# Kernel optimization log

Measured on AMD Instinct MI355X. Metric: run time of the kernel, lower is better.

Reference implementation:

```python
import jax, jax.numpy as jnp
import numpy as np

B, C, H, W = 4, 96, 64, 64
N_STATE, DT_RANK, K = 16, 6, 3


def _layernorm(x, g, b, eps=1e-5):
    m = jnp.mean(x, axis=-1, keepdims=True)
    v = jnp.mean((x - m) ** 2, axis=-1, keepdims=True)
    return (x - m) / jnp.sqrt(v + eps) * g + b


def _grid_sample(img, gx, gy):
    # F.grid_sample: bilinear, align_corners=True, zeros padding; gx,gy in [-1,1], [B,Ho,Wo]
    Bc, Cc, Hi, Wi = img.shape
    fx = (gx + 1.0) * 0.5 * (Wi - 1)
    fy = (gy + 1.0) * 0.5 * (Hi - 1)
    x0 = jnp.floor(fx)
    y0 = jnp.floor(fy)
    wx1 = fx - x0
    wy1 = fy - y0

    def tap(ix, iy, w):
        valid = ((ix >= 0) & (ix < Wi) & (iy >= 0) & (iy < Hi)).astype(img.dtype)
        ic = jnp.clip(ix, 0, Wi - 1).astype(jnp.int32)
        jc = jnp.clip(iy, 0, Hi - 1).astype(jnp.int32)
        v = jax.vmap(lambda im, yy, xx: im[:, yy, xx])(img, jc, ic)  # [B,C,Ho,Wo]
        return v * (w * valid)[:, None, :, :]

    return (tap(x0, y0, (1 - wx1) * (1 - wy1)) + tap(x0 + 1, y0, wx1 * (1 - wy1))
            + tap(x0, y0 + 1, (1 - wx1) * wy1) + tap(x0 + 1, y0 + 1, wx1 * wy1))


def _resize_bilinear(img, Ho, Wo):
    # torch F.interpolate(mode='bilinear', align_corners=False)
    Bc, Cc, Hi, Wi = img.shape

    def src(n_out, n_in):
        s = jnp.maximum((jnp.arange(n_out, dtype=img.dtype) + 0.5) * (n_in / n_out) - 0.5, 0.0)
        i0 = jnp.floor(s).astype(jnp.int32)
        i1 = jnp.minimum(i0 + 1, n_in - 1)
        return i0, i1, s - i0

    y0, y1, wy = src(Ho, Hi)
    x0, x1, wx = src(Wo, Wi)
    row = img[:, :, y0, :] * (1 - wy)[None, None, :, None] + img[:, :, y1, :] * wy[None, None, :, None]
    return row[:, :, :, x0] * (1 - wx) + row[:, :, :, x1] * wx


def _conv_offset(x, conv1_w, conv1_b, ca1_w, ca1_b, ca2_w, ca2_b, ln_g, ln_b, conv2_w):
    Bc, Cc = x.shape[:2]
    p = conv1_w.shape[-1] // 2
    x1 = jax.lax.conv_general_dilated(
        x, conv1_w, (1, 1), [(p, p), (p, p)],
        dimension_numbers=("NCHW", "OIHW", "NCHW"), feature_group_count=Cc
    ) + conv1_b[None, :, None, None]
    xc = jnp.mean(x, axis=(2, 3))  # adaptive_avg_pool2d -> (1,1)
    hid = jax.nn.gelu(xc @ ca1_w.T + ca1_b, approximate=False)
    ca = jax.nn.sigmoid(hid @ ca2_w.T + ca2_b)
    x1 = x1 * ca[:, :, None, None]
    xn = _layernorm(jnp.transpose(x1, (0, 2, 3, 1)), ln_g, ln_b)
    xg = jax.nn.gelu(jnp.transpose(xn, (0, 3, 1, 2)), approximate=False)
    return jnp.einsum("bchw,oc->bohw", xg, conv2_w[:, :, 0, 0])


def _deformable(x, rpe_table, conv1_w, conv1_b, ca1_w, ca1_b, ca2_w, ca2_b, ln_g, ln_b, conv2_w):
    Bc, Cc, Hc, Wc = x.shape
    L = Hc * Wc
    off = _conv_offset(x, conv1_w, conv1_b, ca1_w, ca1_b, ca2_w, ca2_b, ln_g, ln_b, conv2_w)
    offset = off[:, :2]
    de = off[:, 2]
    rng = jnp.array([1.0 / (Hc - 1.0), 1.0 / (Wc - 1.0)], off.dtype).reshape(1, 2, 1, 1)
    offset = jnp.transpose(jnp.tanh(offset) * rng, (0, 2, 3, 1))  # [B,H,W,2] (dy,dx)
    ry = (jnp.linspace(0.5, Hc - 0.5, Hc) / (Hc - 1.0)) * 2.0 - 1.0
    rx = (jnp.linspace(0.5, Wc - 0.5, Wc) / (Wc - 1.0)) * 2.0 - 1.0
    ref = jnp.stack(jnp.meshgrid(ry, rx, indexing="ij"), -1)  # [H,W,2] (y,x)
    pos = offset + ref[None]
    de_index = jnp.tanh(de).reshape(Bc, L)
    path_ref = (jnp.linspace(0.5, L - 0.5, L) / (L - 1.0)) * 2.0 - 1.0
    path_pos = de_index + path_ref[None]
    x_sampled = _grid_sample(x, pos[..., 1], pos[..., 0])
    rpe = jnp.broadcast_to(rpe_table[None], (Bc,) + rpe_table.shape)
    rpe_bias = _resize_bilinear(rpe, Hc, Wc)
    ky = (jnp.linspace(0.0, float(Hc), Hc) / (Hc - 1.0)) * 2.0 - 1.0
    kx = (jnp.linspace(0.0, float(Wc), Wc) / (Wc - 1.0)) * 2.0 - 1.0
    key_grid = jnp.stack(jnp.meshgrid(ky, kx, indexing="ij"), -1)
    disp = (key_grid[None] - pos) * 0.5
    pos_bias = _grid_sample(rpe_bias, disp[..., 1], disp[..., 0])
    xd = (x_sampled + pos_bias).reshape(Bc, Cc, L)
    indices = jnp.argsort(path_pos, axis=-1)  # topk(k=N, largest=False) == ascending argsort
    xs2 = jnp.take_along_axis(xd, indices[:, None, :], axis=2)
    return xs2, indices


def _selective_scan(u, delta, A, Bs, Cs, Dv, delta_bias):
    Bc, KD, L = u.shape
    Kk = Bs.shape[1]
    Dd = KD // Kk
    Ns = A.shape[1]
    delta = jax.nn.softplus(delta + delta_bias[None, :, None])
    dt4 = jnp.moveaxis(delta.reshape(Bc, Kk, Dd, L), 3, 0)
    u4 = jnp.moveaxis(u.reshape(Bc, Kk, Dd, L), 3, 0)
    Bt = jnp.moveaxis(Bs, 3, 0)
    Ct = jnp.moveaxis(Cs, 3, 0)
    A3 = A.reshape(Kk, Dd, Ns)

    @jax.checkpoint
    def step(h, inp):
        dt, ut, bt, ct = inp  # [B,K,D],[B,K,D],[B,K,N],[B,K,N]
        h = jnp.exp(dt[..., None] * A3) * h + (dt * ut)[..., None] * bt[:, :, None, :]
        return h, jnp.einsum("bkdn,bkn->bkd", h, ct)

    h0 = jnp.zeros((Bc, Kk, Dd, Ns), u.dtype)
    _, ys = jax.lax.scan(step, h0, (dt4, u4, Bt, Ct))
    ys = jnp.moveaxis(ys, 0, 3).reshape(Bc, KD, L)
    return ys + u * Dv[None, :, None]


def _forward(x, x_proj_weight, dt_projs_weight, dt_projs_bias, A_logs, Ds_param,
             conv1_w, conv1_b, ca1_w, ca1_b, ca2_w, ca2_b, ln_g, ln_b, conv2_w, rpe_table):
    Bc, Dd, Hc, Wc = x.shape
    L = Hc * Wc
    Kk, _, R = dt_projs_weight.shape
    Ns = A_logs.shape[1]
    xs0 = x.reshape(Bc, Dd, L)
    xs2, indices = _deformable(x, rpe_table, conv1_w, conv1_b, ca1_w, ca1_b, ca2_w, ca2_b, ln_g, ln_b, conv2_w)
    xs = jnp.stack([xs0, xs0[..., ::-1], xs2], axis=1)  # [B,3,D,L]
    x_dbl = jnp.einsum("bkdl,kcd->bkcl", xs, x_proj_weight)
    dts, Bs, Cs = jnp.split(x_dbl, [R, R + Ns], axis=2)
    dts = jnp.einsum("bkrl,kdr->bkdl", dts, dt_projs_weight)
    A = -jnp.exp(A_logs)
    ys = _selective_scan(xs.reshape(Bc, Kk * Dd, L), dts.reshape(Bc, Kk * Dd, L),
                         A, Bs, Cs, Ds_param, dt_projs_bias.reshape(-1))
    ys = ys.reshape(Bc, Kk, Dd, L)
    inv = jnp.argsort(indices, axis=-1)  # inverse permutation (DeformableLayerReverse)
    y2 = jnp.take_along_axis(ys[:, 2], inv[:, None, :], axis=2)
    y = (ys[:, 0] + ys[:, 1][..., ::-1] + y2) / 3.0
    return jnp.transpose(y, (0, 2, 1)).reshape(Bc, Hc, Wc, Dd)


def setup_inputs():
    key = jax.random.key(0)
    ks = jax.random.split(key, 12)
    f = jnp.float32
    return {
        "x": jax.random.normal(ks[0], (B, C, H, W), f),
        "x_proj_weight": jax.random.normal(ks[1], (K, DT_RANK + 2 * N_STATE, C), f) * 0.05,
        "dt_projs_weight": jax.random.normal(ks[2], (K, C, DT_RANK), f) * 0.05,
        "dt_projs_bias": jax.random.normal(ks[3], (K, C), f) * 0.1,
        "A_logs": jnp.tile(jnp.log(jnp.arange(1, N_STATE + 1, dtype=f))[None, :], (K * C, 1)),
        "Ds_param": jnp.ones((K * C,), f),
        "conv1_w": jax.random.normal(ks[4], (C, 1, 9, 9), f) * 0.05,
        "conv1_b": jnp.zeros((C,), f),
        "ca1_w": jax.random.normal(ks[5], (C // 16, C), f) * 0.1,
        "ca1_b": jnp.zeros((C // 16,), f),
        "ca2_w": jax.random.normal(ks[6], (C, C // 16), f) * 0.1,
        "ca2_b": jnp.zeros((C,), f),
        "ln_g": jnp.ones((C,), f),
        "ln_b": jnp.zeros((C,), f),
        "conv2_w": jax.random.normal(ks[7], (3, C, 1, 1), f) * 0.05,
        "rpe_table": jax.random.normal(ks[8], (C, 7, 7), f) * 0.01,
    }


def reference(x, x_proj_weight, dt_projs_weight, dt_projs_bias, A_logs, Ds_param,
              conv1_w, conv1_b, ca1_w, ca1_b, ca2_w, ca2_b, ln_g, ln_b, conv2_w, rpe_table):
    return _forward(x, x_proj_weight, dt_projs_weight, dt_projs_bias, A_logs, Ds_param,
                    conv1_w, conv1_b, ca1_w, ca1_b, ca2_w, ca2_b, ln_g, ln_b, conv2_w, rpe_table)
```

## Files before the change

kernel.cpp:

```cpp
#include <hip/hip_runtime.h>

#define BB 4
#define CC 96
#define HH 64
#define WW 64
#define LL 4096
#define KK 3
#define RR 6
#define NN 16

__device__ __forceinline__ float geluf(float x){
    return 0.5f * x * (1.0f + erff(x * 0.70710678118654752f));
}
__device__ __forceinline__ float softplusf(float x){
    return fmaxf(x, 0.0f) + log1pf(expf(-fabsf(x)));
}
__device__ __forceinline__ float sigmoidf(float x){
    return 1.0f / (1.0f + expf(-x));
}

__global__ __launch_bounds__(256) void k_mean(const float* __restrict__ x, float* __restrict__ xc){
    int bc = blockIdx.x;
    const float* p = x + (size_t)bc * LL;
    float s = 0.f;
    for (int i = threadIdx.x; i < LL; i += 256) s += p[i];
    __shared__ float red[256];
    red[threadIdx.x] = s; __syncthreads();
    for (int st = 128; st > 0; st >>= 1){
        if (threadIdx.x < st) red[threadIdx.x] += red[threadIdx.x + st];
        __syncthreads();
    }
    if (threadIdx.x == 0) xc[bc] = red[0] * (1.0f / LL);
}

__global__ __launch_bounds__(128) void k_ca(const float* __restrict__ xc,
                     const float* __restrict__ w1, const float* __restrict__ b1,
                     const float* __restrict__ w2, const float* __restrict__ b2,
                     float* __restrict__ ca){
    int b = blockIdx.x;
    int t = threadIdx.x;
    __shared__ float hid[CC/16];
    if (t < CC/16){
        float a = b1[t];
        for (int d = 0; d < CC; d++) a += w1[t*CC + d] * xc[b*CC + d];
        hid[t] = geluf(a);
    }
    __syncthreads();
    if (t < CC){
        float a = b2[t];
        #pragma unroll
        for (int i = 0; i < CC/16; i++) a += w2[t*(CC/16) + i] * hid[i];
        ca[b*CC + t] = sigmoidf(a);
    }
}

__global__ __launch_bounds__(256) void k_conv(const float* __restrict__ x, const float* __restrict__ w,
                       const float* __restrict__ bias, const float* __restrict__ ca,
                       float* __restrict__ x1){
    int gid = blockIdx.x * 256 + threadIdx.x;
    int l = gid & (LL-1); int bc = gid >> 12;
    int c = bc % CC; int b = bc / CC;
    int h = l >> 6, wq = l & 63;
    const float* xp = x + (size_t)bc * LL;
    const float* wp = w + c * 81;
    float acc = 0.f;
    #pragma unroll
    for (int ky = 0; ky < 9; ky++){
        int yy = h + ky - 4;
        if (yy < 0 || yy >= HH) continue;
        #pragma unroll
        for (int kx = 0; kx < 9; kx++){
            int xx = wq + kx - 4;
            if (xx < 0 || xx >= WW) continue;
            acc += xp[yy*WW + xx] * wp[ky*9 + kx];
        }
    }
    x1[gid] = (acc + bias[c]) * ca[b*CC + c];
}

__global__ __launch_bounds__(256) void k_rpe(const float* __restrict__ t, float* __restrict__ out){
    int gid = blockIdx.x * 256 + threadIdx.x;
    int l = gid & (LL-1); int c = gid >> 12;
    int h = l >> 6, w = l & 63;
    float sy = fmaxf((h + 0.5f) * (7.0f/64.0f) - 0.5f, 0.f);
    float sx = fmaxf((w + 0.5f) * (7.0f/64.0f) - 0.5f, 0.f);
    int y0 = (int)floorf(sy); int x0 = (int)floorf(sx);
    float wy = sy - (float)y0, wx = sx - (float)x0;
    int y1 = min(y0 + 1, 6), x1i = min(x0 + 1, 6);
    const float* tp = t + c * 49;
    float r0 = tp[y0*7 + x0] * (1.f - wy) + tp[y1*7 + x0] * wy;
    float r1 = tp[y0*7 + x1i] * (1.f - wy) + tp[y1*7 + x1i] * wy;
    out[gid] = r0 * (1.f - wx) + r1 * wx;
}

__global__ __launch_bounds__(256) void k_off(const float* __restrict__ x1,
                      const float* __restrict__ g, const float* __restrict__ bta,
                      const float* __restrict__ w2,
                      float* __restrict__ posy, float* __restrict__ posx, float* __restrict__ path){
    int blk = blockIdx.x;
    int ltile = blk & 63; int b = blk >> 6;
    int lane = threadIdx.x & 63;
    int wg = threadIdx.x >> 6;
    int l = ltile * 64 + lane;
    const float* p = x1 + (size_t)b * CC * LL + l;
    float v[24];
    float s = 0.f, ss = 0.f;
    #pragma unroll
    for (int j = 0; j < 24; j++){
        float t = p[(size_t)(wg*24 + j) * LL];
        v[j] = t; s += t; ss += t*t;
    }
    __shared__ float ls[4][64], lss[4][64];
    ls[wg][lane] = s; lss[wg][lane] = ss;
    __syncthreads();
    s  = ls[0][lane]  + ls[1][lane]  + ls[2][lane]  + ls[3][lane];
    ss = lss[0][lane] + lss[1][lane] + lss[2][lane] + lss[3][lane];
    float m = s * (1.0f/CC);
    float rstd = rsqrtf(ss*(1.0f/CC) - m*m + 1e-5f);
    float a0 = 0.f, a1 = 0.f, a2 = 0.f;
    #pragma unroll
    for (int j = 0; j < 24; j++){
        int c = wg*24 + j;
        float xn = (v[j]-m)*rstd*g[c] + bta[c];
        float xg = geluf(xn);
        a0 = fmaf(w2[c],      xg, a0);
        a1 = fmaf(w2[CC+c],   xg, a1);
        a2 = fmaf(w2[2*CC+c], xg, a2);
    }
    __shared__ float la[3][4][64];
    la[0][wg][lane] = a0; la[1][wg][lane] = a1; la[2][wg][lane] = a2;
    __syncthreads();
    if (wg < 3){
        float a = la[wg][0][lane] + la[wg][1][lane] + la[wg][2][lane] + la[wg][3][lane];
        int h = l >> 6, w = l & 63;
        if (wg == 0)      posy[b*LL + l] = tanhf(a)*(1.0f/63.0f) + ((2*h+1)*(1.0f/63.0f) - 1.0f);
        else if (wg == 1) posx[b*LL + l] = tanhf(a)*(1.0f/63.0f) + ((2*w+1)*(1.0f/63.0f) - 1.0f);
        else              path[b*LL + l] = tanhf(a) + ((l + 0.5f)*(2.0f/4095.0f) - 1.0f);
    }
}

typedef unsigned long long u64s;
__device__ __forceinline__ u64s shflx64(u64s x, int m){
    int lo = __shfl_xor((int)(unsigned)x, m);
    int hi = __shfl_xor((int)(unsigned)(x >> 32), m);
    return ((u64s)(unsigned)hi << 32) | (unsigned)lo;
}
__device__ __forceinline__ void cex(u64s& a, u64s& b, bool up){
    u64s mn = a < b ? a : b;
    u64s mx = a < b ? b : a;
    a = up ? mn : mx;
    b = up ? mx : mn;
}
__global__ __launch_bounds__(1024) void k_sort(const float* __restrict__ path,
                                               int* __restrict__ idx, int* __restrict__ inv){
    int b = blockIdx.x;
    int t = threadIdx.x;
    __shared__ u64s lds[LL];
    u64s v[4];
    #pragma unroll
    for (int r = 0; r < 4; r++){
        int e = t*4 + r;
        unsigned u = __float_as_uint(path[b*LL + e]);
        u ^= (u >> 31) ? 0xFFFFFFFFu : 0x80000000u;
        v[r] = ((u64s)u << 32) | (unsigned)e;
    }
    for (int kk = 2; kk <= LL; kk <<= 1){
        for (int j = kk >> 1; j > 0; j >>= 1){
            if (j >= 256){
                __syncthreads();
                #pragma unroll
                for (int r = 0; r < 4; r++) lds[t*4 + r] = v[r];
                __syncthreads();
                #pragma unroll
                for (int r = 0; r < 4; r++){
                    int e = t*4 + r;
                    u64s pv = lds[e ^ j];
                    bool up    = ((e & kk) == 0);
                    bool lower = ((e & j) == 0);
                    u64s mn = v[r] < pv ? v[r] : pv;
                    u64s mx = v[r] < pv ? pv : v[r];
                    v[r] = (up == lower) ? mn : mx;
                }
            } else if (j >= 4){
                int m = j >> 2;
                #pragma unroll
                for (int r = 0; r < 4; r++){
                    u64s pv = shflx64(v[r], m);
                    bool up    = (((t*4 + r) & kk) == 0);
                    bool lower = ((t & m) == 0);
                    u64s mn = v[r] < pv ? v[r] : pv;
                    u64s mx = v[r] < pv ? pv : v[r];
                    v[r] = (up == lower) ? mn : mx;
                }
            } else if (j == 2){
                bool up = (((t*4) & kk) == 0);
                cex(v[0], v[2], up);
                cex(v[1], v[3], up);
            } else {
                if (kk == 2){
                    cex(v[0], v[1], true);
                    cex(v[2], v[3], false);
                } else {
                    bool up = (((t*4) & kk) == 0);
                    cex(v[0], v[1], up);
                    cex(v[2], v[3], up);
                }
            }
        }
    }
    #pragma unroll
    for (int r = 0; r < 4; r++){
        int e = t*4 + r;
        int id = (int)(unsigned)(v[r] & 0xFFFFFFFFu);
        idx[b*LL + e] = id;
        inv[b*LL + id] = e;
    }
}

__device__ __forceinline__ float bilin0(const float* __restrict__ img, float gx, float gy){
    float fx = (gx + 1.f) * 31.5f;
    float fy = (gy + 1.f) * 31.5f;
    float x0f = floorf(fx), y0f = floorf(fy);
    float wx = fx - x0f, wy = fy - y0f;
    int x0 = (int)x0f, y0 = (int)y0f;
    float acc = 0.f;
    bool vx0 = (x0 >= 0) & (x0 < WW), vx1 = (x0+1 >= 0) & (x0+1 < WW);
    bool vy0 = (y0 >= 0) & (y0 < HH), vy1 = (y0+1 >= 0) & (y0+1 < HH);
    if (vy0 & vx0) acc += img[y0*WW + x0]       * (1.f-wx) * (1.f-wy);
    if (vy0 & vx1) acc += img[y0*WW + x0+1]     * wx       * (1.f-wy);
    if (vy1 & vx0) acc += img[(y0+1)*WW + x0]   * (1.f-wx) * wy;
    if (vy1 & vx1) acc += img[(y0+1)*WW + x0+1] * wx       * wy;
    return acc;
}

__global__ __launch_bounds__(256) void k_sample(const float* __restrict__ x, const float* __restrict__ rpe,
                         const float* __restrict__ posy, const float* __restrict__ posx,
                         float* __restrict__ xd){
    int gid = blockIdx.x * 256 + threadIdx.x;
    int l = gid & (LL-1); int bc = gid >> 12;
    int b = bc / CC; int c = bc % CC;
    float gy = posy[b*LL + l], gx = posx[b*LL + l];
    float v = bilin0(x + (size_t)bc * LL, gx, gy);
    int h = l >> 6, w = l & 63;
    float ky = h * (128.0f/3969.0f) - 1.0f;
    float kx = w * (128.0f/3969.0f) - 1.0f;
    float v2 = bilin0(rpe + (size_t)c * LL, (kx - gx) * 0.5f, (ky - gy) * 0.5f);
    xd[gid] = v + v2;
}

__global__ __launch_bounds__(192, 1) void k_proj(const float* __restrict__ x, const float* __restrict__ xd,
    const int* __restrict__ indices, const float* __restrict__ xpw, const float* __restrict__ dtw,
    const float* __restrict__ dtb, float* __restrict__ u2, float* __restrict__ dt,
    float* __restrict__ Bst, float* __restrict__ Cst){
    int blk = blockIdx.x;
    int ltile = blk & 63; int bk = blk >> 6;
    int k = bk % KK; int b = bk / KK;
    int lane = threadIdx.x & 63;
    int w = threadIdx.x >> 6;
    const float* __restrict__ Wk = xpw + k*38*CC;
    int l = ltile * 64 + lane;
    int srcl = (k == 0) ? l : (k == 1 ? (LL-1-l) : indices[b*LL + l]);
    const float* xp = (k == 2 ? xd : x) + (size_t)b * CC * LL + srcl;

    __shared__ float vsh[CC*64];
    #pragma unroll
    for (int j = 0; j < 32; j++){
        int d = w*32 + j;
        vsh[d*64 + lane] = xp[(size_t)d * LL];
    }
    __syncthreads();

    if (w == 0){
        float acc[RR];
        #pragma unroll
        for (int i = 0; i < RR; i++) acc[i] = 0.f;
        for (int d = 0; d < CC; d++){
            float vv = vsh[d*64 + lane];
            #pragma unroll
            for (int i = 0; i < RR; i++) acc[i] = fmaf(Wk[i*CC + d], vv, acc[i]);
        }
        const float* __restrict__ Dw = dtw + k*CC*RR;
        const float* __restrict__ Db = dtb + k*CC;
        float* dtp = dt + (size_t)bk * CC * LL + l;
        #pragma unroll 8
        for (int d = 0; d < CC; d++){
            float sdt = Db[d];
            #pragma unroll
            for (int r = 0; r < RR; r++) sdt = fmaf(acc[r], Dw[d*RR + r], sdt);
            dtp[(size_t)d * LL] = softplusf(sdt);
        }
    } else if (w == 1){
        float acc[NN];
        #pragma unroll
        for (int i = 0; i < NN; i++) acc[i] = 0.f;
        for (int d = 0; d < CC; d++){
            float vv = vsh[d*64 + lane];
            #pragma unroll
            for (int i = 0; i < NN; i++) acc[i] = fmaf(Wk[(RR + i)*CC + d], vv, acc[i]);
        }
        size_t base = ((size_t)bk * LL + l) * NN;
        #pragma unroll
        for (int q = 0; q < 4; q++){
            float4 o; o.x = acc[q*4]; o.y = acc[q*4+1]; o.z = acc[q*4+2]; o.w = acc[q*4+3];
            *(float4*)(Bst + base + q*4) = o;
        }
    } else {
        float acc[NN];
        #pragma unroll
        for (int i = 0; i < NN; i++) acc[i] = 0.f;
        for (int d = 0; d < CC; d++){
            float vv = vsh[d*64 + lane];
            #pragma unroll
            for (int i = 0; i < NN; i++) acc[i] = fmaf(Wk[(RR + NN + i)*CC + d], vv, acc[i]);
        }
        size_t base = ((size_t)bk * LL + l) * NN;
        #pragma unroll
        for (int q = 0; q < 4; q++){
            float4 o; o.x = acc[q*4]; o.y = acc[q*4+1]; o.z = acc[q*4+2]; o.w = acc[q*4+3];
            *(float4*)(Cst + base + q*4) = o;
        }
        if (k == 2){
            float* up = u2 + (size_t)b * CC * LL + l;
            #pragma unroll 8
            for (int d = 0; d < CC; d++) up[(size_t)d * LL] = vsh[d*64 + lane];
        }
    }
}

#define SEG 128
#define TL 32
template<int KIND>
__device__ __forceinline__ void scan_body(int b, int d, const float* __restrict__ usrc,
    const float* __restrict__ dt, const float* __restrict__ Bst, const float* __restrict__ Cst,
    const float* __restrict__ Alog, const float* __restrict__ Ds, float* __restrict__ ys,
    float* sA, float* sB, float* sCin, float* sdt, float* su){
    int bk = b * KK + KIND;
    int tid = threadIdx.x;
    int ng = tid & 3;
    int seg = tid >> 2;
    int t0 = seg * TL;

    const float4 A4 = *(const float4*)(Alog + (KIND*CC + d)*NN + 4*ng);
    float A[4] = { -__expf(A4.x), -__expf(A4.y), -__expf(A4.z), -__expf(A4.w) };
    float Dv = Ds[KIND*CC + d];

    const float* dtp = dt + ((size_t)bk * CC + d) * LL + t0;
    const float* ub = (KIND == 1)
        ? usrc + ((size_t)b*CC + d) * LL + (LL-4-t0)
        : usrc + ((size_t)b*CC + d) * LL + t0;
    const float* Bp = Bst + ((size_t)bk * LL + t0) * NN + 4*ng;
    const float* Cp = Cst + ((size_t)bk * LL + t0) * NN + 4*ng;
    float* yp = ys + ((size_t)bk * CC + d) * LL + t0;

    float Ap[4] = {1.f,1.f,1.f,1.f}, h[4] = {0.f,0.f,0.f,0.f};
    for (int t = 0; t < TL; t += 4){
        float4 dq = *(const float4*)(dtp + t);
        float4 uq = (KIND == 1) ? *(const float4*)(ub - t) : *(const float4*)(ub + t);
        float dd[4] = {dq.x, dq.y, dq.z, dq.w};
        float uu[4];
        if (KIND == 1){ uu[0]=uq.w; uu[1]=uq.z; uu[2]=uq.y; uu[3]=uq.x; }
        else          { uu[0]=uq.x; uu[1]=uq.y; uu[2]=uq.z; uu[3]=uq.w; }
        if (ng == 0){
            *(float4*)(sdt + t0 + t) = dq;
            float4 us; us.x = uu[0]; us.y = uu[1]; us.z = uu[2]; us.w = uu[3];
            *(float4*)(su + t0 + t) = us;
        }
        #pragma unroll
        for (int i = 0; i < 4; i++){
            float4 Bq = *(const float4*)(Bp + (t+i)*NN);
            float du = dd[i] * uu[i];
            float bb[4] = {Bq.x, Bq.y, Bq.z, Bq.w};
            #pragma unroll
            for (int j = 0; j < 4; j++){
                float a = __expf(dd[i] * A[j]);
                Ap[j] *= a;
                h[j] = fmaf(a, h[j], du * bb[j]);
            }
        }
    }

    #pragma unroll
    for (int j = 0; j < 4; j++){
        sA[seg*16 + 4*ng + j] = Ap[j];
        sB[seg*16 + 4*ng + j] = h[j];
    }
    __syncthreads();
    if (tid < 16){
        float c = 0.f;
        for (int sg = 0; sg < SEG; sg++){
            sCin[sg*16 + tid] = c;
            c = fmaf(sA[sg*16 + tid], c, sB[sg*16 + tid]);
        }
    }
    __syncthreads();
    float hc[4];
    #pragma unroll
    for (int j = 0; j < 4; j++) hc[j] = sCin[seg*16 + 4*ng + j];

    for (int t = 0; t < TL; t += 4){
        float4 dq = *(const float4*)(sdt + t0 + t);
        float4 us = *(const float4*)(su + t0 + t);
        float dd[4] = {dq.x, dq.y, dq.z, dq.w};
        float uu[4] = {us.x, us.y, us.z, us.w};
        float yo[4];
        #pragma unroll
        for (int i = 0; i < 4; i++){
            float4 Bq = *(const float4*)(Bp + (t+i)*NN);
            float4 Cq = *(const float4*)(Cp + (t+i)*NN);
            float du = dd[i] * uu[i];
            float bb[4] = {Bq.x, Bq.y, Bq.z, Bq.w};
            float cc[4] = {Cq.x, Cq.y, Cq.z, Cq.w};
            float p = 0.f;
            #pragma unroll
            for (int j = 0; j < 4; j++){
                float a = __expf(dd[i] * A[j]);
                hc[j] = fmaf(a, hc[j], du * bb[j]);
                p = fmaf(hc[j], cc[j], p);
            }
            p += __shfl_xor(p, 1);
            p += __shfl_xor(p, 2);
            yo[i] = fmaf(uu[i], Dv, p);
        }
        if (ng == 0){
            float4 o; o.x = yo[0]; o.y = yo[1]; o.z = yo[2]; o.w = yo[3];
            *(float4*)(yp + t) = o;
        }
    }
}

__global__ __launch_bounds__(512) void k_scan_all(const float* __restrict__ x, const float* __restrict__ u2,
    const float* __restrict__ dt, const float* __restrict__ Bst, const float* __restrict__ Cst,
    const float* __restrict__ Alog, const float* __restrict__ Ds, float* __restrict__ ys){
    __shared__ float sA[SEG*16];
    __shared__ float sB[SEG*16];
    __shared__ float sCin[SEG*16];
    __shared__ float sdt[LL];
    __shared__ float su[LL];
    int blk = blockIdx.x;
    int k = blk / (BB*CC);
    int r = blk % (BB*CC);
    int d = r % CC; int b = r / CC;
    if (k == 0)      scan_body<0>(b, d, x,  dt, Bst, Cst, Alog, Ds, ys, sA, sB, sCin, sdt, su);
    else if (k == 1) scan_body<1>(b, d, x,  dt, Bst, Cst, Alog, Ds, ys, sA, sB, sCin, sdt, su);
    else             scan_body<2>(b, d, u2, dt, Bst, Cst, Alog, Ds, ys, sA, sB, sCin, sdt, su);
}

__global__ __launch_bounds__(256) void k_comb(const float* __restrict__ ys, const int* __restrict__ inv,
                                              float* __restrict__ out){
    int tile = blockIdx.x & 63; int b = blockIdx.x >> 6;
    int l0 = tile * 64;
    __shared__ float t0[CC * 65];
    __shared__ int invs[64];
    if (threadIdx.x < 64) invs[threadIdx.x] = inv[b*LL + l0 + threadIdx.x];
    __syncthreads();
    const float* y0p = ys + (size_t)(b*KK + 0) * CC * LL;
    const float* y1p = ys + (size_t)(b*KK + 1) * CC * LL;
    const float* y2p = ys + (size_t)(b*KK + 2) * CC * LL;
    for (int it = 0; it < 24; it++){
        int e = it * 256 + threadIdx.x;
        int li = e & 63; int c = e >> 6;
        int l = l0 + li;
        float v = y0p[(size_t)c*LL + l] + y1p[(size_t)c*LL + (LL-1-l)] + y2p[(size_t)c*LL + invs[li]];
        t0[c*65 + li] = v * (1.0f/3.0f);
    }
    __syncthreads();
    for (int it = 0; it < 24; it++){
        int e = it * 256 + threadIdx.x;
        int c = e % CC; int li = e / CC;
        out[((size_t)b*LL + l0 + li) * CC + c] = t0[c*65 + li];
    }
}

extern "C" void kernel_launch(void* const* d_in, const int* in_sizes, int n_in,
                              void* d_out, int out_size, void* d_ws, size_t ws_size,
                              hipStream_t stream){
    const float* x    = (const float*)d_in[0];
    const float* xpw  = (const float*)d_in[1];
    const float* dtw  = (const float*)d_in[2];
    const float* dtb  = (const float*)d_in[3];
    const float* Alog = (const float*)d_in[4];
    const float* Ds   = (const float*)d_in[5];
    const float* c1w  = (const float*)d_in[6];
    const float* c1b  = (const float*)d_in[7];
    const float* ca1w = (const float*)d_in[8];
    const float* ca1b = (const float*)d_in[9];
    const float* ca2w = (const float*)d_in[10];
    const float* ca2b = (const float*)d_in[11];
    const float* lng  = (const float*)d_in[12];
    const float* lnb  = (const float*)d_in[13];
    const float* c2w  = (const float*)d_in[14];
    const float* rpet = (const float*)d_in[15];
    float* out = (float*)d_out;

    float* ws   = (float*)d_ws;
    float* xc   = ws;
    float* ca   = xc + 384;
    float* x1   = ca + 384;
    float* rpe  = x1 + (size_t)BB*CC*LL;
    float* posy = rpe + (size_t)CC*LL;
    float* posx = posy + (size_t)BB*LL;
    float* path = posx + (size_t)BB*LL;
    float* xd   = path + (size_t)BB*LL;
    int*   idx  = (int*)(xd + (size_t)BB*CC*LL);
    int*   inv  = idx + (size_t)BB*LL;
    float* u2   = (float*)(inv + (size_t)BB*LL);
    float* dtA  = u2 + (size_t)BB*CC*LL;
    float* Bst  = dtA + (size_t)BB*KK*CC*LL;
    float* Cst  = Bst + (size_t)BB*KK*LL*NN;
    float* ysA  = Cst + (size_t)BB*KK*LL*NN;

    k_mean  <<<BB*CC, 256, 0, stream>>>(x, xc);
    k_ca    <<<BB, 128, 0, stream>>>(xc, ca1w, ca1b, ca2w, ca2b, ca);
    k_conv  <<<(BB*CC*LL)/256, 256, 0, stream>>>(x, c1w, c1b, ca, x1);
    k_rpe   <<<(CC*LL)/256, 256, 0, stream>>>(rpet, rpe);
    k_off   <<<BB*64, 256, 0, stream>>>(x1, lng, lnb, c2w, posy, posx, path);
    k_sort  <<<BB, 1024, 0, stream>>>(path, idx, inv);
    k_sample<<<(BB*CC*LL)/256, 256, 0, stream>>>(x, rpe, posy, posx, xd);
    k_proj  <<<BB*KK*64, 192, 0, stream>>>(x, xd, idx, xpw, dtw, dtb, u2, dtA, Bst, Cst);
    k_scan_all<<<KK*BB*CC, 512, 0, stream>>>(x, u2, dtA, Bst, Cst, Alog, Ds, ysA);
    k_comb  <<<BB*64, 256, 0, stream>>>(ysA, inv, out);
}
```

Measured before the change: 351.5 us.

## Parallelize scan segment carry combine with wave shuffles and trim shared memory

Replaces the serial 128-step carry propagation, done by 16 threads, with a parallel prefix scan. Each of 8 waves handles 2 state channels, combining pairs of segments and then using shuffle-up over 64 lanes. Shared arrays get padded row strides to avoid bank conflicts. The u values are no longer staged in shared memory and are re-read from global memory in the second pass. The main cost removed is the long serial dependency chain between the two scan passes, and the smaller LDS footprint may also allow more blocks per CU. The trade-off is extra global reloads of u.

```diff
diff --git a/kernel.cpp b/kernel.cpp
--- a/kernel.cpp
+++ b/kernel.cpp
@@ -329,11 +329,13 @@
 
 #define SEG 128
 #define TL 32
+#define SROW 17
+#define DROW 36
 template<int KIND>
 __device__ __forceinline__ void scan_body(int b, int d, const float* __restrict__ usrc,
     const float* __restrict__ dt, const float* __restrict__ Bst, const float* __restrict__ Cst,
     const float* __restrict__ Alog, const float* __restrict__ Ds, float* __restrict__ ys,
-    float* sA, float* sB, float* sCin, float* sdt, float* su){
+    float* sA, float* sB, float* sdt){
     int bk = b * KK + KIND;
     int tid = threadIdx.x;
     int ng = tid & 3;
@@ -360,11 +362,7 @@
         float uu[4];
         if (KIND == 1){ uu[0]=uq.w; uu[1]=uq.z; uu[2]=uq.y; uu[3]=uq.x; }
         else          { uu[0]=uq.x; uu[1]=uq.y; uu[2]=uq.z; uu[3]=uq.w; }
-        if (ng == 0){
-            *(float4*)(sdt + t0 + t) = dq;
-            float4 us; us.x = uu[0]; us.y = uu[1]; us.z = uu[2]; us.w = uu[3];
-            *(float4*)(su + t0 + t) = us;
-        }
+        if (ng == 0) *(float4*)(sdt + seg*DROW + t) = dq;
         #pragma unroll
         for (int i = 0; i < 4; i++){
             float4 Bq = *(const float4*)(Bp + (t+i)*NN);
@@ -381,27 +379,47 @@
 
     #pragma unroll
     for (int j = 0; j < 4; j++){
-        sA[seg*16 + 4*ng + j] = Ap[j];
-        sB[seg*16 + 4*ng + j] = h[j];
-    }
-    __syncthreads();
-    if (tid < 16){
-        float c = 0.f;
-        for (int sg = 0; sg < SEG; sg++){
-            sCin[sg*16 + tid] = c;
-            c = fmaf(sA[sg*16 + tid], c, sB[sg*16 + tid]);
+        sA[seg*SROW + 4*ng + j] = Ap[j];
+        sB[seg*SROW + 4*ng + j] = h[j];
+    }
+    __syncthreads();
+    {
+        int wv = tid >> 6;
+        int lane = tid & 63;
+        #pragma unroll
+        for (int nn = 0; nn < 2; nn++){
+            int n = 2*wv + nn;
+            float a1 = sA[(2*lane)*SROW + n],   b1 = sB[(2*lane)*SROW + n];
+            float a2 = sA[(2*lane+1)*SROW + n], b2 = sB[(2*lane+1)*SROW + n];
+            float ca = a1 * a2;
+            float cb = fmaf(a2, b1, b2);
+            #pragma unroll
+            for (int off = 1; off < 64; off <<= 1){
+                float ta = __shfl_up(ca, off);
+                float tb = __shfl_up(cb, off);
+                if (lane >= off){
+                    cb = fmaf(ca, tb, cb);
+                    ca *= ta;
+                }
+            }
+            float cb_prev = __shfl_up(cb, 1);
+            if (lane == 0) cb_prev = 0.f;
+            sA[(2*lane)*SROW + n]   = cb_prev;
+            sA[(2*lane+1)*SROW + n] = fmaf(a1, cb_prev, b1);
         }
     }
     __syncthreads();
     float hc[4];
     #pragma unroll
-    for (int j = 0; j < 4; j++) hc[j] = sCin[seg*16 + 4*ng + j];
+    for (int j = 0; j < 4; j++) hc[j] = sA[seg*SROW + 4*ng + j];
 
     for (int t = 0; t < TL; t += 4){
-        float4 dq = *(const float4*)(sdt + t0 + t);
-        float4 us = *(const float4*)(su + t0 + t);
+        float4 dq = *(const float4*)(sdt + seg*DROW + t);
+        float4 uq = (KIND == 1) ? *(const float4*)(ub - t) : *(const float4*)(ub + t);
         float dd[4] = {dq.x, dq.y, dq.z, dq.w};
-        float uu[4] = {us.x, us.y, us.z, us.w};
+        float uu[4];
+        if (KIND == 1){ uu[0]=uq.w; uu[1]=uq.z; uu[2]=uq.y; uu[3]=uq.x; }
+        else          { uu[0]=uq.x; uu[1]=uq.y; uu[2]=uq.z; uu[3]=uq.w; }
         float yo[4];
         #pragma unroll
         for (int i = 0; i < 4; i++){
@@ -431,18 +449,16 @@
 __global__ __launch_bounds__(512) void k_scan_all(const float* __restrict__ x, const float* __restrict__ u2,
     const float* __restrict__ dt, const float* __restrict__ Bst, const float* __restrict__ Cst,
     const float* __restrict__ Alog, const float* __restrict__ Ds, float* __restrict__ ys){
-    __shared__ float sA[SEG*16];
-    __shared__ float sB[SEG*16];
-    __shared__ float sCin[SEG*16];
-    __shared__ float sdt[LL];
-    __shared__ float su[LL];
+    __shared__ float sA[SEG*SROW];
+    __shared__ float sB[SEG*SROW];
+    __shared__ float sdt[SEG*DROW];
     int blk = blockIdx.x;
     int k = blk / (BB*CC);
     int r = blk % (BB*CC);
     int d = r % CC; int b = r / CC;
-    if (k == 0)      scan_body<0>(b, d, x,  dt, Bst, Cst, Alog, Ds, ys, sA, sB, sCin, sdt, su);
-    else if (k == 1) scan_body<1>(b, d, x,  dt, Bst, Cst, Alog, Ds, ys, sA, sB, sCin, sdt, su);
-    else             scan_body<2>(b, d, u2, dt, Bst, Cst, Alog, Ds, ys, sA, sB, sCin, sdt, su);
+    if (k == 0)      scan_body<0>(b, d, x,  dt, Bst, Cst, Alog, Ds, ys, sA, sB, sdt);
+    else if (k == 1) scan_body<1>(b, d, x,  dt, Bst, Cst, Alog, Ds, ys, sA, sB, sdt);
+    else             scan_body<2>(b, d, u2, dt, Bst, Cst, Alog, Ds, ys, sA, sB, sdt);
 }
 
 __global__ __launch_bounds__(256) void k_comb(const float* __restrict__ ys, const int* __restrict__ inv,
```

Result: no change. 349.4 us (-0.6%).
